# Kernel tuning notes

Measured on AMD Instinct MI355X. Metric: run time of the kernel, lower is better.

## Reference

```python
import jax, jax.numpy as jnp
import numpy as np

B, L, E, H, W = 2, 8192, 1024, 16, 128
HD = E // H  # 64


def setup_inputs() -> dict:
    key = jax.random.key(0)
    ks = jax.random.split(key, 9)
    s = 1.0 / np.sqrt(E)
    inp = {"x": jax.random.normal(ks[0], (B, L, E), jnp.float32)}
    for i, n in enumerate(["Wq", "Wk", "Wv", "Wo"]):
        inp[n] = jax.random.uniform(ks[1 + i], (E, E), jnp.float32, -s, s)
    for i, n in enumerate(["bq", "bk", "bv", "bo"]):
        inp[n] = jax.random.uniform(ks[5 + i], (E,), jnp.float32, -s, s)
    return inp


def _skew_prob(p, w):
    # (..., w, 2w+1) -> (..., w, 3w) with row i right-shifted by i:
    # out[..., i, i+j] = p[..., i, j]  (zeros elsewhere)
    lead = p.shape[:-2]
    M, Lc = p.shape[-2], p.shape[-1]
    p = jnp.pad(p, [(0, 0)] * len(lead) + [(0, 0), (0, M + 1)])
    p = p.reshape(*lead, M * (Lc + M + 1))[..., :-M].reshape(*lead, M, M + Lc)
    return p[..., :-1]


def _sliding_attend(q, k, v, w):
    # q,k,v: (b,h,l,d); banded attention, window w on each side (2w+1 diagonals)
    b, h, l, d = q.shape
    c = l // w
    qc = q.reshape(b, h, c, w, d)
    # per-chunk key/value windows of 3w tokens (w halo each side, zero padded)
    idx = jnp.arange(c)[:, None] * w + jnp.arange(3 * w)[None, :]  # (c, 3w)
    kw = jnp.pad(k, ((0, 0), (0, 0), (w, w), (0, 0)))[:, :, idx]  # (b,h,c,3w,d)
    s = jnp.einsum('bhcqd,bhckd->bhcqk', qc, kw)  # (b,h,c,w,3w)
    # extract band: band[i, j] = s[i, i+j], j in [0, 2w] (offset d = j - w)
    gidx = (jnp.arange(w)[:, None] + jnp.arange(2 * w + 1)[None, :])[None, None, None]
    band = jnp.take_along_axis(s, gidx, axis=-1).reshape(b, h, l, 2 * w + 1)
    # mask out-of-range positions (matches the module's edge -inf loop)
    pos = jnp.arange(l)[:, None] + (jnp.arange(2 * w + 1) - w)[None, :]
    band = jnp.where((pos >= 0) & (pos < l), band, -jnp.inf)
    prob = jax.nn.softmax(band / np.sqrt(d), axis=-1)  # scale by sqrt(head_dim)
    vw = jnp.pad(v, ((0, 0), (0, 0), (w, w), (0, 0)))[:, :, idx]  # (b,h,c,3w,d)
    p3 = _skew_prob(prob.reshape(b, h, c, w, 2 * w + 1), w)  # (b,h,c,w,3w)
    ctx = jnp.einsum('bhcqk,bhckd->bhcqd', p3, vw)
    return ctx.reshape(b, h, l, d)


def reference(x, Wq, Wk, Wv, Wo, bq, bk, bv, bo):
    q = (x @ Wq.T + bq).reshape(B, L, H, HD).transpose(0, 2, 1, 3)
    k = (x @ Wk.T + bk).reshape(B, L, H, HD).transpose(0, 2, 1, 3)
    v = (x @ Wv.T + bv).reshape(B, L, H, HD).transpose(0, 2, 1, 3)
    ctx = _sliding_attend(q, k, v, W)
    ctx = ctx.transpose(0, 2, 1, 3).reshape(B, L, E)
    return ctx @ Wo.T + bo
```

## Files before the change

### kernel.cpp

```cpp
#include <hip/hip_runtime.h>
#include <math.h>

#define B_SZ  2
#define L_SEQ 8192
#define EMB   1024
#define NH    16
#define HDIM  64
#define WIN   128
#define MROWS (B_SZ*L_SEQ)

typedef __attribute__((ext_vector_type(8))) _Float16 f16x8;
typedef __attribute__((ext_vector_type(4))) _Float16 f16x4;
typedef __attribute__((ext_vector_type(4))) float f32x4;

__device__ __forceinline__ void gload16(const void* g, void* l) {
    __builtin_amdgcn_global_load_lds(
        (const __attribute__((address_space(1))) unsigned int*)g,
        (__attribute__((address_space(3))) unsigned int*)l, 16, 0, 0);
}

__global__ __launch_bounds__(256)
void round_all(const float* __restrict__ x,
               const float* __restrict__ wq, const float* __restrict__ wk,
               const float* __restrict__ wv, const float* __restrict__ wo,
               _Float16* __restrict__ xf, _Float16* __restrict__ q16,
               _Float16* __restrict__ k16, _Float16* __restrict__ v16,
               _Float16* __restrict__ o16)
{
    const size_t NX = (size_t)MROWS * EMB, NW = (size_t)EMB * EMB;
    size_t gid = ((size_t)blockIdx.x * 256 + threadIdx.x) * 4;
    const float* src; _Float16* dst; size_t off;
    if (gid < NX)               { src = x;  dst = xf;  off = gid; }
    else if (gid < NX + NW)     { src = wq; dst = q16; off = gid - NX; }
    else if (gid < NX + 2*NW)   { src = wk; dst = k16; off = gid - NX - 2*NW + NW; }
    else if (gid < NX + 3*NW)   { src = wv; dst = v16; off = gid - NX - 2*NW; }
    else                        { src = wo; dst = o16; off = gid - NX - 3*NW; }
    float4 v = *(const float4*)(src + off);
    f16x4 o;
    o[0] = (_Float16)v.x; o[1] = (_Float16)v.y;
    o[2] = (_Float16)v.z; o[3] = (_Float16)v.w;
    *(f16x4*)(dst + off) = o;
}


#define STAGE_HT(ptr_, tb_, op_, h_, kt_)                                      \
    {                                                                          \
        char* d_ = smem + (op_) * 65536 + ((kt_) & 1) * 32768 + (h_) * 16384 + ldst; \
        const _Float16* s_ = (ptr_) + ((size_t)((tb_) + (h_) * 128 + srow6)) * 1024 + (kt_) * 64 + gch; \
        gload16(s_, d_);                                                       \
        gload16(s_ + 64 * 1024, d_ + 8192);                                    \
    }

#define DSREAD_A(qr_)                                                          \
    _Pragma("unroll")                                                          \
    for (int i_ = 0; i_ < 4; ++i_) {                                           \
        const int ro_ = (qr_) * 8192 + (i_ * 16 + frow) * 128;                 \
        af[i_][0] = *(const f16x8*)(Ab + ro_ + sb0);                           \
        af[i_][1] = *(const f16x8*)(Ab + ro_ + sb1);                           \
    }

#define DSREAD_B(qc_)                                                          \
    _Pragma("unroll")                                                          \
    for (int j_ = 0; j_ < 2; ++j_) {                                           \
        const int ro_ = (brow + (qc_) * 32 + j_ * 16 + frow) * 128;            \
        bf[j_][0] = *(const f16x8*)(Bb + ro_ + sb0);                           \
        bf[j_][1] = *(const f16x8*)(Bb + ro_ + sb1);                           \
    }

#define MFMA16(qr_, qc_)                                                       \
    __builtin_amdgcn_s_setprio(1);                                             \
    _Pragma("unroll")                                                          \
    for (int ks_ = 0; ks_ < 2; ++ks_)                                          \
        _Pragma("unroll")                                                      \
        for (int i_ = 0; i_ < 4; ++i_)                                         \
            _Pragma("unroll")                                                  \
            for (int j_ = 0; j_ < 2; ++j_)                                     \
                acc[(qr_) * 4 + i_][(qc_) * 2 + j_] =                          \
                    __builtin_amdgcn_mfma_f32_16x16x32_f16(                    \
                        af[i_][ks_], bf[j_][ks_],                              \
                        acc[(qr_) * 4 + i_][(qc_) * 2 + j_], 0, 0, 0);         \
    __builtin_amdgcn_s_setprio(0);

#define BARM()                                                                 \
    asm volatile("" ::: "memory");                                             \
    __builtin_amdgcn_s_barrier();                                              \
    asm volatile("" ::: "memory");

#define GEMM8_CORE(Aptr, Bptr)                                                 \
    const int t = threadIdx.x;                                                 \
    const int wave = t >> 6, lane = t & 63;                                    \
    const int wr = wave >> 2, wc = wave & 3;                                   \
    const int frow = lane & 15, quad = lane >> 4;                              \
    const int srow6 = t >> 3;                                                  \
    const int gch = ((t & 7) ^ (srow6 & 7)) * 8;                               \
    const int ldst = t * 16;                                                   \
    const int sb0 = (quad ^ (frow & 7)) * 16, sb1 = sb0 ^ 64;                  \
    const int brow = (wc & 1) * 64;                                            \
    f32x4 acc[8][4] = {};                                                      \
    f16x8 af[4][2], bf[2][2];                                                  \
    STAGE_HT(Aptr, bm, 0, 0, 0) STAGE_HT(Aptr, bm, 0, 1, 0)                    \
    STAGE_HT(Bptr, bn, 1, 0, 0) STAGE_HT(Bptr, bn, 1, 1, 0)                    \
    for (int kt = 0; kt < 16; ++kt) {                                          \
        const char* Ab = smem + (kt & 1) * 32768 + wr * 16384;                 \
        const char* Bb = smem + 65536 + (kt & 1) * 32768 + (wc >> 1) * 16384;  \
        if (kt < 15) {                                                         \
            STAGE_HT(Aptr, bm, 0, 0, kt + 1)                                   \
            asm volatile("s_waitcnt vmcnt(2)" ::: "memory");                   \
        } else {                                                               \
            asm volatile("s_waitcnt vmcnt(0)" ::: "memory");                   \
        }                                                                      \
        BARM()                                                                 \
        DSREAD_A(0) DSREAD_B(0)                  \
        MFMA16(0, 0)                                                           \
        DSREAD_B(1)                            \
        if (kt < 15) STAGE_HT(Aptr, bm, 0, 1, kt + 1)                          \
        BARM()                                                                 \
        MFMA16(0, 1)                                                           \
        DSREAD_A(1)                                                            \
        if (kt < 15) STAGE_HT(Bptr, bn, 1, 0, kt + 1)                          \
        BARM()                                                                 \
        MFMA16(1, 1)                                                           \
        DSREAD_B(0)                                \
        if (kt < 15) STAGE_HT(Bptr, bn, 1, 1, kt + 1)                          \
        BARM()                                                                 \
        MFMA16(1, 0)                                                           \
        BARM()                                                                 \
    }

__global__ __launch_bounds__(512, 2)
void gemm_qkv(const _Float16* __restrict__ X,
              const _Float16* __restrict__ Wq, const _Float16* __restrict__ Wk,
              const _Float16* __restrict__ Wv,
              const float* __restrict__ bq, const float* __restrict__ bk,
              const float* __restrict__ bv,
              _Float16* __restrict__ qf, _Float16* __restrict__ kf,
              _Float16* __restrict__ vtf)
{
    __shared__ __attribute__((aligned(16))) char smem[131072];

    const int id = blockIdx.x;
    const int row = (id / 96) * 8 + (id & 7);
    const int colq = (id >> 3) % 12;
    const int wsel = colq >> 2;
    const int bm = row * 256, bn = (colq & 3) * 256;
    const _Float16* Bw = wsel == 0 ? Wq : wsel == 1 ? Wk : Wv;
    const float* bias = wsel == 0 ? bq : wsel == 1 ? bk : bv;
    const float scale = wsel == 0 ? 0.125f : 1.0f;

    GEMM8_CORE(X, Bw)

    char* Cw = smem + wave * 8192;
    const int bb = bm >> 13;
    const int l0 = (bm & (L_SEQ - 1)) + wr * 128;
    const int h = (bn >> 6) + wc;
    if (wsel < 2) {
        _Float16* dst = wsel == 0 ? qf : kf;
        const size_t hb = ((size_t)(bb * NH + h)) * L_SEQ * HDIM;
        #pragma unroll
        for (int ih = 0; ih < 2; ++ih) {
            asm volatile("" ::: "memory");
            #pragma unroll
            for (int i = 0; i < 4; ++i)
                #pragma unroll
                for (int j = 0; j < 4; ++j) {
                    const int lc = j * 16 + frow;
                    const float bvv = bias[bn + wc * 64 + lc];
                    #pragma unroll
                    for (int r = 0; r < 4; ++r) {
                        const int lr = i * 16 + quad * 4 + r;
                        const int bo = lr * 128 + ((lc * 2) ^ ((lr & 7) << 4));
                        *(_Float16*)(Cw + bo) = (_Float16)((acc[ih * 4 + i][j][r] + bvv) * scale);
                    }
                }
            asm volatile("" ::: "memory");
            #pragma unroll
            for (int p = 0; p < 8; ++p) {
                const int idx = p * 64 + lane;
                const int lr = idx >> 3, seg = idx & 7;
                const int bo = lr * 128 + ((seg * 16) ^ ((lr & 7) << 4));
                uint4 v = *(const uint4*)(Cw + bo);
                *(uint4*)&dst[hb + (size_t)(l0 + ih * 64 + lr) * HDIM + seg * 8] = v;
            }
        }
    } else {
        const size_t hb = ((size_t)(bb * NH + h)) * HDIM * L_SEQ;
        #pragma unroll
        for (int ih = 0; ih < 2; ++ih) {
            asm volatile("" ::: "memory");
            #pragma unroll
            for (int i = 0; i < 4; ++i)
                #pragma unroll
                for (int j = 0; j < 4; ++j) {
                    const int lc = j * 16 + frow;
                    const float bvv = bias[bn + wc * 64 + lc];
                    #pragma unroll
                    for (int r = 0; r < 4; ++r) {
                        const int lr = i * 16 + quad * 4 + r;
                        const int bo = lc * 128 + ((lr * 2) ^ ((lc & 7) << 4));
                        *(_Float16*)(Cw + bo) = (_Float16)(acc[ih * 4 + i][j][r] + bvv);
                    }
                }
            asm volatile("" ::: "memory");
            #pragma unroll
            for (int p = 0; p < 8; ++p) {
                const int idx = p * 64 + lane;
                const int dc = idx >> 3, sl = idx & 7;
                const int bo = dc * 128 + ((sl * 16) ^ ((dc & 7) << 4));
                uint4 v = *(const uint4*)(Cw + bo);
                *(uint4*)&vtf[hb + (size_t)dc * L_SEQ + (l0 + ih * 64 + sl * 8)] = v;
            }
        }
    }
}

__global__ __launch_bounds__(512, 2)
void gemm_out(const _Float16* __restrict__ A, const _Float16* __restrict__ Bwm,
              const float* __restrict__ bias, float* __restrict__ C)
{
    constexpr int N = EMB;
    __shared__ __attribute__((aligned(16))) char smem[131072];

    const int id = blockIdx.x;
    const int row = (id / 32) * 8 + (id & 7);
    const int bm = row * 256, bn = ((id >> 3) & 3) * 256;

    GEMM8_CORE(A, Bwm)

    #pragma unroll
    for (int i = 0; i < 8; ++i) {
        int m0 = bm + wr * 128 + i * 16 + quad * 4;
        #pragma unroll
        for (int j = 0; j < 4; ++j) {
            int n = bn + wc * 64 + j * 16 + frow;
            float bvv = bias[n];
            #pragma unroll
            for (int r = 0; r < 4; ++r)
                C[(size_t)(m0 + r) * N + n] = acc[i][j][r] + bvv;
        }
    }
}

__global__ __launch_bounds__(512)
void attn_mfma(const _Float16* __restrict__ qf, const _Float16* __restrict__ kf,
               const _Float16* __restrict__ vtf, _Float16* __restrict__ cf)
{
    __shared__ _Float16 Kf[2][4096], Vf[2][4096];
    __shared__ _Float16 Ps[8][16 * 72];

    const int t = threadIdx.x;
    const int wave = t >> 6, lane = t & 63;
    const int col = lane & 15, quad = lane >> 4;
    const int bh = blockIdx.y;
    const int q0 = blockIdx.x * 128;
    const int oo = wave * 16;

    f16x8 qfr[2];
    {
        size_t qidx = ((size_t)bh * L_SEQ + q0 + oo + col) * HDIM + quad * 8;
        qfr[0] = *(const f16x8*)(qf + qidx);
        qfr[1] = *(const f16x8*)(qf + qidx + 32);
    }

    f32x4 o[4] = {};
    float lsum[4] = {};

    const int srow = t >> 3, sc = t & 7;
    _Float16* Pw = Ps[wave];

    const int ktlo = (q0 == 0) ? 2 : 0;
    const int kthi = (q0 == L_SEQ - 128) ? 4 : 6;

#define STAGE_KV(kt_, bsel_)                                                   \
    {                                                                          \
        const int p0s = q0 - WIN + (kt_) * 64;                                 \
        const int gq = sc ^ (srow & 7);                                        \
        size_t kgi = ((size_t)bh * L_SEQ + p0s + srow) * HDIM + gq * 8;        \
        size_t vgi = ((size_t)bh * HDIM + srow) * L_SEQ + p0s + gq * 8;        \
        gload16(kf + kgi, (char*)&Kf[bsel_][0] + t * 16);                      \
        gload16(vtf + vgi, (char*)&Vf[bsel_][0] + t * 16);                     \
    }

    STAGE_KV(ktlo, 0)

    for (int kt = ktlo; kt < kthi; kt++) {
        const int p0 = q0 - WIN + kt * 64;
        const int cb = (kt - ktlo) & 1;
        if (kt + 1 < kthi) {
            STAGE_KV(kt + 1, cb ^ 1)
            asm volatile("s_waitcnt vmcnt(2)" ::: "memory");
        } else {
            asm volatile("s_waitcnt vmcnt(0)" ::: "memory");
        }
        __builtin_amdgcn_s_barrier();
        asm volatile("" ::: "memory");

        const char* Kb = (const char*)&Kf[cb][0];
        const char* Vb = (const char*)&Vf[cb][0];

        const int relp = kt * 64 - WIN - oo;
        if (relp >= -191 && relp <= 143) {
            f32x4 s[4] = {};
            #pragma unroll
            for (int ks = 0; ks < 2; ks++)
                #pragma unroll
                for (int n = 0; n < 4; n++) {
                    int off = (n * 16 + col) * 128 + (((ks * 4 + quad) ^ (col & 7)) * 16);
                    f16x8 kfr = *(const f16x8*)(Kb + off);
                    s[n] = __builtin_amdgcn_mfma_f32_16x16x32_f16(qfr[ks], kfr, s[n], 0, 0, 0);
                }
            if (relp < -113 || relp > 65) {
                const int rowb = q0 + oo + quad * 4;
                #pragma unroll
                for (int n = 0; n < 4; n++)
                    #pragma unroll
                    for (int r = 0; r < 4; r++) {
                        int dlt = (p0 + n * 16 + col) - (rowb + r);
                        if (dlt < -WIN || dlt > WIN) s[n][r] = -3e38f;
                    }
            }
            #pragma unroll
            for (int n = 0; n < 4; n++)
                #pragma unroll
                for (int r = 0; r < 4; r++) {
                    float pv = __expf(s[n][r]);
                    lsum[r] += pv;
                    Pw[(quad * 4 + r) * 72 + n * 16 + col] = (_Float16)pv;
                }
            #pragma unroll
            for (int ks = 0; ks < 2; ks++) {
                f16x8 pfr = *(const f16x8*)&Pw[col * 72 + ks * 32 + quad * 8];
                #pragma unroll
                for (int n = 0; n < 4; n++) {
                    int off = (n * 16 + col) * 128 + (((ks * 4 + quad) ^ (col & 7)) * 16);
                    f16x8 vfr = *(const f16x8*)(Vb + off);
                    o[n] = __builtin_amdgcn_mfma_f32_16x16x32_f16(pfr, vfr, o[n], 0, 0, 0);
                }
            }
        }
        asm volatile("" ::: "memory");
        __builtin_amdgcn_s_barrier();
        asm volatile("" ::: "memory");
    }

    #pragma unroll
    for (int x = 1; x < 16; x <<= 1)
        #pragma unroll
        for (int r = 0; r < 4; r++)
            lsum[r] += __shfl_xor(lsum[r], x, 64);

    const int b = bh >> 4, h = bh & 15;
    #pragma unroll
    for (int r = 0; r < 4; r++) {
        float inv = 1.0f / lsum[r];
        int q = q0 + oo + quad * 4 + r;
        size_t base = ((size_t)b * L_SEQ + q) * EMB + h * HDIM;
        #pragma unroll
        for (int n = 0; n < 4; n++)
            cf[base + n * 16 + col] = (_Float16)(o[n][r] * inv);
    }
}

extern "C" void kernel_launch(void* const* d_in, const int* in_sizes, int n_in,
                              void* d_out, int out_size, void* d_ws, size_t ws_size,
                              hipStream_t stream) {
    const float* x  = (const float*)d_in[0];
    const float* Wq = (const float*)d_in[1];
    const float* Wk = (const float*)d_in[2];
    const float* Wv = (const float*)d_in[3];
    const float* Wo = (const float*)d_in[4];
    const float* bq = (const float*)d_in[5];
    const float* bk = (const float*)d_in[6];
    const float* bv = (const float*)d_in[7];
    const float* bo = (const float*)d_in[8];
    float* out = (float*)d_out;

    const size_t per = (size_t)B_SZ * NH * L_SEQ * HDIM;
    _Float16* w16 = (_Float16*)d_ws;
    _Float16* xf   = w16;
    _Float16* qf   = w16 + per;
    _Float16* kf   = w16 + 2 * per;
    _Float16* vtf  = w16 + 3 * per;
    _Float16* cf   = w16 + 4 * per;
    _Float16* wq16 = w16 + 5 * per;
    _Float16* wk16 = wq16 + 1048576;
    _Float16* wv16 = wq16 + 2 * 1048576;
    _Float16* wo16 = wq16 + 3 * 1048576;

    const int nround = (MROWS * EMB + 4 * EMB * EMB) / 1024;
    round_all<<<nround, dim3(256), 0, stream>>>(x, Wq, Wk, Wv, Wo, xf, wq16, wk16, wv16, wo16);

    gemm_qkv<<<768, dim3(512), 0, stream>>>(xf, wq16, wk16, wv16, bq, bk, bv, qf, kf, vtf);

    attn_mfma<<<dim3(L_SEQ / 128, B_SZ * NH), dim3(512), 0, stream>>>(qf, kf, vtf, cf);

    gemm_out<<<256, dim3(512), 0, stream>>>(cf, wo16, bo, out);
}
```

Before: 325.6 us.

## Compute transposed scores to keep probabilities in registers for PV MFMA

The QK^T MFMA now computes S transposed by swapping its operands, so each lane's accumulator layout matches the B-operand layout of a 16x16x16 MFMA. The probabilities then feed the PV product straight from registers instead of round-tripping through a per-wave LDS buffer. The row sum reduces to a single value per lane, and the output is written as packed 4-wide f16 stores. This removes the LDS writes and reads for P and the shared buffer, at the cost of using twice as many smaller K=16 MFMAs with narrower V fragment loads.

```diff
diff --git a/kernel.cpp b/kernel.cpp
--- a/kernel.cpp
+++ b/kernel.cpp
@@ -245,7 +245,6 @@
                const _Float16* __restrict__ vtf, _Float16* __restrict__ cf)
 {
     __shared__ _Float16 Kf[2][4096], Vf[2][4096];
-    __shared__ _Float16 Ps[8][16 * 72];
 
     const int t = threadIdx.x;
     const int wave = t >> 6, lane = t & 63;
@@ -262,10 +261,9 @@
     }
 
     f32x4 o[4] = {};
-    float lsum[4] = {};
+    float lsum = 0.0f;
 
     const int srow = t >> 3, sc = t & 7;
-    _Float16* Pw = Ps[wave];
 
     const int ktlo = (q0 == 0) ? 2 : 0;
     const int kthi = (q0 == L_SEQ - 128) ? 4 : 6;
@@ -299,41 +297,42 @@
 
         const int relp = kt * 64 - WIN - oo;
         if (relp >= -191 && relp <= 143) {
-            f32x4 s[4] = {};
+            f32x4 sT[4] = {};
             #pragma unroll
             for (int ks = 0; ks < 2; ks++)
                 #pragma unroll
                 for (int n = 0; n < 4; n++) {
                     int off = (n * 16 + col) * 128 + (((ks * 4 + quad) ^ (col & 7)) * 16);
                     f16x8 kfr = *(const f16x8*)(Kb + off);
-                    s[n] = __builtin_amdgcn_mfma_f32_16x16x32_f16(qfr[ks], kfr, s[n], 0, 0, 0);
+                    sT[n] = __builtin_amdgcn_mfma_f32_16x16x32_f16(kfr, qfr[ks], sT[n], 0, 0, 0);
                 }
             if (relp < -113 || relp > 65) {
-                const int rowb = q0 + oo + quad * 4;
+                const int qrow = q0 + oo + col;
                 #pragma unroll
                 for (int n = 0; n < 4; n++)
                     #pragma unroll
                     for (int r = 0; r < 4; r++) {
-                        int dlt = (p0 + n * 16 + col) - (rowb + r);
-                        if (dlt < -WIN || dlt > WIN) s[n][r] = -3e38f;
+                        int dlt = (p0 + n * 16 + quad * 4 + r) - qrow;
+                        if (dlt < -WIN || dlt > WIN) sT[n][r] = -3e38f;
                     }
             }
+            f16x4 pT[4];
             #pragma unroll
             for (int n = 0; n < 4; n++)
                 #pragma unroll
                 for (int r = 0; r < 4; r++) {
-                    float pv = __expf(s[n][r]);
-                    lsum[r] += pv;
-                    Pw[(quad * 4 + r) * 72 + n * 16 + col] = (_Float16)pv;
-                }
-            #pragma unroll
-            for (int ks = 0; ks < 2; ks++) {
-                f16x8 pfr = *(const f16x8*)&Pw[col * 72 + ks * 32 + quad * 8];
+                    float pv = __expf(sT[n][r]);
+                    lsum += pv;
+                    pT[n][r] = (_Float16)pv;
+                }
+            #pragma unroll
+            for (int m = 0; m < 4; m++) {
                 #pragma unroll
                 for (int n = 0; n < 4; n++) {
-                    int off = (n * 16 + col) * 128 + (((ks * 4 + quad) ^ (col & 7)) * 16);
-                    f16x8 vfr = *(const f16x8*)(Vb + off);
-                    o[n] = __builtin_amdgcn_mfma_f32_16x16x32_f16(pfr, vfr, o[n], 0, 0, 0);
+                    int off = (m * 16 + col) * 128 +
+                              (((2 * n + (quad >> 1)) ^ (col & 7)) * 16) + (quad & 1) * 8;
+                    f16x4 vfr = *(const f16x4*)(Vb + off);
+                    o[m] = __builtin_amdgcn_mfma_f32_16x16x16f16(vfr, pT[n], o[m], 0, 0, 0);
                 }
             }
         }
@@ -342,21 +341,18 @@
         asm volatile("" ::: "memory");
     }
 
+    lsum += __shfl_xor(lsum, 16, 64);
+    lsum += __shfl_xor(lsum, 32, 64);
+    const float inv = 1.0f / lsum;
+
+    const int b = bh >> 4, h = bh & 15;
+    const size_t base = ((size_t)b * L_SEQ + q0 + oo + col) * EMB + h * HDIM;
     #pragma unroll
-    for (int x = 1; x < 16; x <<= 1)
+    for (int m = 0; m < 4; m++) {
+        f16x4 ov;
         #pragma unroll
-        for (int r = 0; r < 4; r++)
-            lsum[r] += __shfl_xor(lsum[r], x, 64);
-
-    const int b = bh >> 4, h = bh & 15;
-    #pragma unroll
-    for (int r = 0; r < 4; r++) {
-        float inv = 1.0f / lsum[r];
-        int q = q0 + oo + quad * 4 + r;
-        size_t base = ((size_t)b * L_SEQ + q) * EMB + h * HDIM;
-        #pragma unroll
-        for (int n = 0; n < 4; n++)
-            cf[base + n * 16 + col] = (_Float16)(o[n][r] * inv);
+        for (int r = 0; r < 4; r++) ov[r] = (_Float16)(o[m][r] * inv);
+        *(f16x4*)&cf[base + m * 16 + quad * 4] = ov;
     }
 }
 
```

Result: faster. 314.3 us (-3.5%).
